# Kernel optimization log

Measured on AMD Instinct MI355X. Metric: run time of the kernel, lower is better.

## Reference

```python
import jax, jax.numpy as jnp
import numpy as np

NB_CLASSES = 1024
SZ_EMBED = 128
N_SAMPLES = 262144
MRG = 0.1
ALPHA = 32.0


def l2_norm(x):
    # matches torch l2_norm: divide by sqrt(sum(x^2, dim=1) + 1e-12)
    return x / jnp.sqrt(jnp.sum(x * x, axis=1, keepdims=True) + 1e-12)


def setup_inputs() -> dict:
    key = jax.random.key(0)
    k1, k2, k3 = jax.random.split(key, 3)
    X = jax.random.normal(k1, (N_SAMPLES, SZ_EMBED), dtype=jnp.float32)
    proxies = jax.random.normal(k2, (NB_CLASSES, SZ_EMBED), dtype=jnp.float32)
    T = jax.random.randint(k3, (N_SAMPLES,), 0, NB_CLASSES)
    return {"X": X, "proxies": proxies, "T": T}


def reference(X, proxies, T):
    # cosine similarities: [N, C]
    cos = l2_norm(X) @ l2_norm(proxies).T
    # on-device one-hot replaces the numpy binarize roundtrip
    P_one_hot = jax.nn.one_hot(T, NB_CLASSES, dtype=cos.dtype)  # [N, C]
    pos_exp_w = jnp.exp(-ALPHA * (cos - MRG)) * P_one_hot
    neg_exp_w = jnp.exp(ALPHA * (cos + MRG)) * (1.0 - P_one_hot)
    P_sim_sum = pos_exp_w.sum(axis=0)  # [C]
    N_sim_sum = neg_exp_w.sum(axis=0)  # [C]
    num_valid = (P_one_hot.sum(axis=0) != 0).sum().astype(cos.dtype)
    pos_term = jnp.where(
        num_valid > 0,
        jnp.log1p(P_sim_sum).sum() / jnp.maximum(num_valid, 1.0),
        jnp.zeros((), cos.dtype),
    )
    neg_term = jnp.log1p(N_sim_sum).sum() / NB_CLASSES
    loss = pos_term + neg_term
    return jnp.stack([loss, pos_term, neg_term])
```

## Files before the change

kernel.cpp:

```cpp
#include <hip/hip_runtime.h>
#include <math.h>

#define NB_CLASSES 1024
#define SZ_EMBED 128
#define N_SAMPLES 262144
#define MTILE 64
#define CTILE 64
#define NBLOCKS (N_SAMPLES / MTILE)
#define XSTRIDE 136

typedef __bf16 v8bf __attribute__((ext_vector_type(8)));
typedef float v4f __attribute__((ext_vector_type(4)));

#define EXP_A 46.16624130844683f
#define EXP_B 4.616624130844683f

#define SMEM_BYTES 36096

__device__ __forceinline__ unsigned short f2bf(float f) {
    union { float f; unsigned u; } v; v.f = f;
    unsigned u = v.u;
    unsigned rounding = 0x7FFFu + ((u >> 16) & 1u);
    return (unsigned short)((u + rounding) >> 16);
}
__device__ __forceinline__ float bfbits_lo(unsigned u) {
    union { unsigned u; float f; } v; v.u = u << 16; return v.f;
}
__device__ __forceinline__ float bfbits_hi(unsigned u) {
    union { unsigned u; float f; } v; v.u = u & 0xffff0000u; return v.f;
}

__global__ __launch_bounds__(256) void norm_proxies_kernel(
    const float* __restrict__ proxies, unsigned short* __restrict__ pn,
    float* __restrict__ pg) {
    if (blockIdx.x < 8) pg[blockIdx.x * 256 + threadIdx.x] = 0.f;
    int wv = threadIdx.x >> 6;
    int lane = threadIdx.x & 63;
    int row = blockIdx.x * 4 + wv;
    const float* src = proxies + (size_t)row * SZ_EMBED + lane * 2;
    float2 x = *(const float2*)src;
    float ss = x.x * x.x + x.y * x.y;
    #pragma unroll
    for (int off = 32; off; off >>= 1) ss += __shfl_xor(ss, off);
    float inv = rsqrtf(ss + 1e-12f);
    unsigned pk = (unsigned)f2bf(x.x * inv) | ((unsigned)f2bf(x.y * inv) << 16);
    *(unsigned*)(pn + (size_t)row * SZ_EMBED + lane * 2) = pk;
}

__global__ __launch_bounds__(256) void main_kernel(
    const float* __restrict__ X, const int* __restrict__ T,
    const unsigned short* __restrict__ Pn,
    float* __restrict__ partial_neg, float* __restrict__ pos_g,
    float* __restrict__ negd_g) {
    __shared__ __align__(16) char smem[SMEM_BYTES];
    unsigned short* xtile = (unsigned short*)smem;
    float (*psum)[4] = (float(*)[4])(smem + 17408);
    float (*dsum)[4] = (float(*)[4])(smem + 18432);
    int* tT = (int*)(smem + 19456);

    const int t = threadIdx.x;
    const int lane = t & 63;
    const int wv = t >> 6;
    const int quad = lane >> 4;
    const int l15 = lane & 15;
    const int sample_base = blockIdx.x * MTILE;
    const int row = t >> 2, part = t & 3;
    const char* PnB = (const char*)Pn;

#define STAGE(tc, b) do {                                                      \
        char* lb_ = smem + ((b) ? 0 : 19712) + wv * 4096;                      \
        _Pragma("unroll")                                                      \
        for (int c_ = 0; c_ < 4; ++c_) {                                       \
            int rw_ = c_ * 4 + (lane >> 4);                                    \
            const char* g_ = PnB + ((size_t)((tc) * 64 + wv * 16 + rw_)) * 256 \
                             + (((lane & 15) * 16) ^ ((rw_ & 7) << 4));        \
            __builtin_amdgcn_global_load_lds(                                  \
                (__attribute__((address_space(1))) const void*)g_,             \
                (__attribute__((address_space(3))) void*)(lb_ + c_ * 1024),    \
                16, 0, 0);                                                     \
        }                                                                      \
    } while (0)

    STAGE(0, 0);

    {
        const float4* src = (const float4*)(X + (size_t)(sample_base + row) * SZ_EMBED + part * 32);
        float4 r[8];
        float ss = 0.f;
        #pragma unroll
        for (int j = 0; j < 8; ++j) {
            r[j] = src[j];
            ss += r[j].x * r[j].x + r[j].y * r[j].y + r[j].z * r[j].z + r[j].w * r[j].w;
        }
        psum[row][part] = ss;
        if (t < MTILE) tT[t] = T[sample_base + t];
        __syncthreads();
        float inv = rsqrtf(psum[row][0] + psum[row][1] + psum[row][2] + psum[row][3] + 1e-12f);
        unsigned short* dst = xtile + row * XSTRIDE + part * 32;
        #pragma unroll
        for (int j = 0; j < 8; ++j) {
            uint2 pk;
            pk.x = (unsigned)f2bf(r[j].x * inv) | ((unsigned)f2bf(r[j].y * inv) << 16);
            pk.y = (unsigned)f2bf(r[j].z * inv) | ((unsigned)f2bf(r[j].w * inv) << 16);
            *(uint2*)(dst + j * 4) = pk;
        }
        int lbl = tT[row];
        const unsigned short* prow = Pn + (size_t)lbl * SZ_EMBED + part * 32;
        float d = 0.f;
        #pragma unroll
        for (int j = 0; j < 4; ++j) {
            uint4 pv = *(const uint4*)(prow + j * 8);
            float4 xa = r[2 * j], xb = r[2 * j + 1];
            d += bfbits_lo(pv.x) * xa.x + bfbits_hi(pv.x) * xa.y;
            d += bfbits_lo(pv.y) * xa.z + bfbits_hi(pv.y) * xa.w;
            d += bfbits_lo(pv.z) * xb.x + bfbits_hi(pv.z) * xb.y;
            d += bfbits_lo(pv.w) * xb.z + bfbits_hi(pv.w) * xb.w;
        }
        dsum[row][part] = d * inv;
        __syncthreads();
        if (part == 0) {
            int lbl2 = tT[row];
            float dd = dsum[row][0] + dsum[row][1] + dsum[row][2] + dsum[row][3];
            float dp = __builtin_amdgcn_exp2f(fmaf(dd, -EXP_A, EXP_B));
            float dn = __builtin_amdgcn_exp2f(fmaf(dd,  EXP_A, EXP_B));
            atomicAdd(&pos_g[lbl2], dp);
            atomicAdd(&negd_g[lbl2], dn);
        }
    }

    v8bf afrag[4][4];
    #pragma unroll
    for (int ri = 0; ri < 4; ++ri)
        #pragma unroll
        for (int kc = 0; kc < 4; ++kc)
            afrag[ri][kc] = *(const v8bf*)(xtile + (ri * 16 + l15) * XSTRIDE + kc * 32 + quad * 8);

    __syncthreads();

    float* nrow = partial_neg + (size_t)blockIdx.x * NB_CLASSES + wv * 16 + l15;
    const int bswz = ((l15 & 7) << 4);
    const int browoff = (wv * 16 + l15) * 256;

    #pragma unroll
    for (int ct = 0; ct < NB_CLASSES / CTILE; ++ct) {
        const int cur = ct & 1;
        if (ct < NB_CLASSES / CTILE - 1) STAGE(ct + 1, cur ^ 1);

        const char* bbase = smem + (cur ? 0 : 19712) + browoff;
        v8bf bfrag[4];
        #pragma unroll
        for (int kc = 0; kc < 4; ++kc)
            bfrag[kc] = *(const v8bf*)(bbase + ((kc * 64 + quad * 16) ^ bswz));

        v4f zero = {0.f, 0.f, 0.f, 0.f};
        v4f acc[4] = {zero, zero, zero, zero};
        #pragma unroll
        for (int kc = 0; kc < 4; ++kc)
            #pragma unroll
            for (int ri = 0; ri < 4; ++ri)
                acc[ri] = __builtin_amdgcn_mfma_f32_16x16x32_bf16(afrag[ri][kc], bfrag[kc], acc[ri], 0, 0, 0);

        float e[16];
        #pragma unroll
        for (int ri = 0; ri < 4; ++ri)
            #pragma unroll
            for (int r = 0; r < 4; ++r)
                e[ri * 4 + r] = __builtin_amdgcn_exp2f(fmaf(acc[ri][r], EXP_A, EXP_B));
        #pragma unroll
        for (int s = 8; s; s >>= 1)
            #pragma unroll
            for (int j = 0; j < s; ++j)
                e[j] += e[j + s];
        float v = e[0];
        v += __shfl_xor(v, 16);
        v += __shfl_xor(v, 32);
        if (quad == 0) nrow[ct * CTILE] = v;

        __syncthreads();
    }
#undef STAGE
}

__global__ __launch_bounds__(256) void row_reduce_kernel(float* __restrict__ partial_neg) {
    const int t = threadIdx.x;
    const int g = blockIdx.x >> 2, q = blockIdx.x & 3;
    float* base = partial_neg + (size_t)g * 64 * NB_CLASSES + q * 256 + t;
    float s = 0.f;
    #pragma unroll 8
    for (int r = 0; r < 64; ++r) s += base[(size_t)r * NB_CLASSES];
    base[0] = s;
}

__global__ __launch_bounds__(256) void finalize_kernel(
    const float* __restrict__ partial_neg, const float* __restrict__ pos_g,
    const float* __restrict__ negd_g, float* __restrict__ out) {
    int t = threadIdx.x;
    float4 ns = {0.f, 0.f, 0.f, 0.f};
    #pragma unroll 8
    for (int r = 0; r < 64; ++r) {
        float4 vn = *(const float4*)(partial_neg + (size_t)r * 64 * NB_CLASSES + 4 * t);
        ns.x += vn.x; ns.y += vn.y; ns.z += vn.z; ns.w += vn.w;
    }
    float4 nd = *(const float4*)(negd_g + 4 * t);
    ns.x -= nd.x; ns.y -= nd.y; ns.z -= nd.z; ns.w -= nd.w;
    float4 ps = *(const float4*)(pos_g + 4 * t);
    float lp_pos = log1pf(ps.x) + log1pf(ps.y) + log1pf(ps.z) + log1pf(ps.w);
    float lp_neg = log1pf(ns.x) + log1pf(ns.y) + log1pf(ns.z) + log1pf(ns.w);
    float valid = (ps.x != 0.f) + (ps.y != 0.f) + (ps.z != 0.f) + (ps.w != 0.f);
    #pragma unroll
    for (int off = 32; off; off >>= 1) {
        lp_pos += __shfl_xor(lp_pos, off);
        lp_neg += __shfl_xor(lp_neg, off);
        valid  += __shfl_xor(valid, off);
    }
    __shared__ float s[3][4];
    int wv = t >> 6, lane = t & 63;
    if (lane == 0) { s[0][wv] = lp_pos; s[1][wv] = lp_neg; s[2][wv] = valid; }
    __syncthreads();
    if (t == 0) {
        float P = s[0][0] + s[0][1] + s[0][2] + s[0][3];
        float Ng = s[1][0] + s[1][1] + s[1][2] + s[1][3];
        float V = s[2][0] + s[2][1] + s[2][2] + s[2][3];
        float pos_term = (V > 0.f) ? (P / fmaxf(V, 1.f)) : 0.f;
        float neg_term = Ng / (float)NB_CLASSES;
        out[0] = pos_term + neg_term;
        out[1] = pos_term;
        out[2] = neg_term;
    }
}

extern "C" void kernel_launch(void* const* d_in, const int* in_sizes, int n_in,
                              void* d_out, int out_size, void* d_ws, size_t ws_size,
                              hipStream_t stream) {
    const float* X = (const float*)d_in[0];
    const float* proxies = (const float*)d_in[1];
    const int* T = (const int*)d_in[2];
    float* out = (float*)d_out;

    char* ws = (char*)d_ws;
    unsigned short* Pn = (unsigned short*)ws;
    float* pos_g = (float*)(ws + (size_t)NB_CLASSES * SZ_EMBED * sizeof(unsigned short));
    float* negd_g = pos_g + NB_CLASSES;
    float* partial_neg = negd_g + NB_CLASSES;

    norm_proxies_kernel<<<NB_CLASSES / 4, 256, 0, stream>>>(proxies, Pn, pos_g);
    main_kernel<<<NBLOCKS, 256, 0, stream>>>(X, T, Pn, partial_neg, pos_g, negd_g);
    row_reduce_kernel<<<256, 256, 0, stream>>>(partial_neg);
    finalize_kernel<<<1, 256, 0, stream>>>(partial_neg, pos_g, negd_g, out);
}
```

Measured before the change: 289.1 us.

## Replace per-tile block barrier with vmcnt waits and pack exp-sum adds

Drops the __syncthreads at the end of each class-tile iteration. In its place, each wave waits on its own outstanding global loads with s_waitcnt vmcnt, and a sched_barrier keeps the compiler from moving code across that wait. The exponentials are now grouped into float2 vectors so the tree reduction can use packed fp32 adds, roughly halving the add instruction count. The change only stays correct if each wave stages and reads only its own part of the double-buffered LDS tile; otherwise removing the barrier opens a race between waves.

After: 283.8 us. No clear change (-1.8%).

```diff
diff --git a/kernel.cpp b/kernel.cpp
--- a/kernel.cpp
+++ b/kernel.cpp
@@ -11,6 +11,7 @@
 
 typedef __bf16 v8bf __attribute__((ext_vector_type(8)));
 typedef float v4f __attribute__((ext_vector_type(4)));
+typedef float v2f __attribute__((ext_vector_type(2)));
 
 #define EXP_A 46.16624130844683f
 #define EXP_B 4.616624130844683f
@@ -144,7 +145,13 @@
     #pragma unroll
     for (int ct = 0; ct < NB_CLASSES / CTILE; ++ct) {
         const int cur = ct & 1;
-        if (ct < NB_CLASSES / CTILE - 1) STAGE(ct + 1, cur ^ 1);
+        if (ct < NB_CLASSES / CTILE - 1) {
+            STAGE(ct + 1, cur ^ 1);
+            asm volatile("s_waitcnt vmcnt(4)" ::: "memory");
+        } else {
+            asm volatile("s_waitcnt vmcnt(0)" ::: "memory");
+        }
+        __builtin_amdgcn_sched_barrier(0);
 
         const char* bbase = smem + (cur ? 0 : 19712) + browoff;
         v8bf bfrag[4];
@@ -160,23 +167,25 @@
             for (int ri = 0; ri < 4; ++ri)
                 acc[ri] = __builtin_amdgcn_mfma_f32_16x16x32_bf16(afrag[ri][kc], bfrag[kc], acc[ri], 0, 0, 0);
 
-        float e[16];
-        #pragma unroll
-        for (int ri = 0; ri < 4; ++ri)
+        v2f e2[8];
+        #pragma unroll
+        for (int ri = 0; ri < 4; ++ri) {
+            float a0 = __builtin_amdgcn_exp2f(fmaf(acc[ri][0], EXP_A, EXP_B));
+            float a1 = __builtin_amdgcn_exp2f(fmaf(acc[ri][1], EXP_A, EXP_B));
+            float a2 = __builtin_amdgcn_exp2f(fmaf(acc[ri][2], EXP_A, EXP_B));
+            float a3 = __builtin_amdgcn_exp2f(fmaf(acc[ri][3], EXP_A, EXP_B));
+            e2[ri * 2]     = (v2f){a0, a1};
+            e2[ri * 2 + 1] = (v2f){a2, a3};
+        }
+        #pragma unroll
+        for (int s2 = 4; s2; s2 >>= 1)
             #pragma unroll
-            for (int r = 0; r < 4; ++r)
-                e[ri * 4 + r] = __builtin_amdgcn_exp2f(fmaf(acc[ri][r], EXP_A, EXP_B));
-        #pragma unroll
-        for (int s = 8; s; s >>= 1)
-            #pragma unroll
-            for (int j = 0; j < s; ++j)
-                e[j] += e[j + s];
-        float v = e[0];
+            for (int j = 0; j < s2; ++j)
+                e2[j] += e2[j + s2];
+        float v = e2[0].x + e2[0].y;
         v += __shfl_xor(v, 16);
         v += __shfl_xor(v, 32);
         if (quad == 0) nrow[ct * CTILE] = v;
-
-        __syncthreads();
     }
 #undef STAGE
 }
```

## Split warps 2x2 over rows/classes and move tile barrier before staging

Applied to the files above, without the earlier changes.

Each wave now computes a 32-row by 32-class sub-tile instead of all 64 rows by 16 classes, which halves the A-fragment registers per wave and doubles partial_neg rows per block. The row-reduce and finalize kernels are resized to the 128-row partial groups. The per-tile barrier moves to the start of the loop, preceded by an explicit vmcnt wait, and the exp-sum uses paired float adds. The intent is lower register pressure, better occupancy and less sync overhead, at the cost of twice as much partial-sum memory traffic.

New measurement: 299.4 us. 1.04x slower.

```diff
diff --git a/kernel.cpp b/kernel.cpp
--- a/kernel.cpp
+++ b/kernel.cpp
@@ -11,6 +11,7 @@
 
 typedef __bf16 v8bf __attribute__((ext_vector_type(8)));
 typedef float v4f __attribute__((ext_vector_type(4)));
+typedef float v2f __attribute__((ext_vector_type(2)));
 
 #define EXP_A 46.16624130844683f
 #define EXP_B 4.616624130844683f
@@ -63,6 +64,8 @@
     const int wv = t >> 6;
     const int quad = lane >> 4;
     const int l15 = lane & 15;
+    const int wr = wv >> 1;
+    const int wc = wv & 1;
     const int sample_base = blockIdx.x * MTILE;
     const int row = t >> 2, part = t & 3;
     const char* PnB = (const char*)Pn;
@@ -128,55 +131,59 @@
         }
     }
 
-    v8bf afrag[4][4];
-    #pragma unroll
-    for (int ri = 0; ri < 4; ++ri)
+    v8bf afrag[2][4];
+    #pragma unroll
+    for (int ri = 0; ri < 2; ++ri)
         #pragma unroll
         for (int kc = 0; kc < 4; ++kc)
-            afrag[ri][kc] = *(const v8bf*)(xtile + (ri * 16 + l15) * XSTRIDE + kc * 32 + quad * 8);
+            afrag[ri][kc] = *(const v8bf*)(xtile + (wr * 32 + ri * 16 + l15) * XSTRIDE + kc * 32 + quad * 8);
 
     __syncthreads();
 
-    float* nrow = partial_neg + (size_t)blockIdx.x * NB_CLASSES + wv * 16 + l15;
+    float* nrow = partial_neg + (size_t)(blockIdx.x * 2 + wr) * NB_CLASSES + wc * 32 + l15;
     const int bswz = ((l15 & 7) << 4);
-    const int browoff = (wv * 16 + l15) * 256;
+    const int brow0 = (wc * 32 + l15) * 256;
 
     #pragma unroll
     for (int ct = 0; ct < NB_CLASSES / CTILE; ++ct) {
         const int cur = ct & 1;
+        asm volatile("s_waitcnt vmcnt(2)" ::: "memory");
+        __builtin_amdgcn_s_barrier();
+        __builtin_amdgcn_sched_barrier(0);
         if (ct < NB_CLASSES / CTILE - 1) STAGE(ct + 1, cur ^ 1);
-
-        const char* bbase = smem + (cur ? 0 : 19712) + browoff;
-        v8bf bfrag[4];
-        #pragma unroll
-        for (int kc = 0; kc < 4; ++kc)
-            bfrag[kc] = *(const v8bf*)(bbase + ((kc * 64 + quad * 16) ^ bswz));
-
-        v4f zero = {0.f, 0.f, 0.f, 0.f};
-        v4f acc[4] = {zero, zero, zero, zero};
-        #pragma unroll
-        for (int kc = 0; kc < 4; ++kc)
+        __builtin_amdgcn_sched_barrier(0);
+
+        const char* bbase = smem + (cur ? 0 : 19712);
+        #pragma unroll
+        for (int ci = 0; ci < 2; ++ci) {
+            const char* bb = bbase + brow0 + ci * 4096;
+            v8bf bfrag[4];
             #pragma unroll
-            for (int ri = 0; ri < 4; ++ri)
-                acc[ri] = __builtin_amdgcn_mfma_f32_16x16x32_bf16(afrag[ri][kc], bfrag[kc], acc[ri], 0, 0, 0);
-
-        float e[16];
-        #pragma unroll
-        for (int ri = 0; ri < 4; ++ri)
+            for (int kc = 0; kc < 4; ++kc)
+                bfrag[kc] = *(const v8bf*)(bb + ((kc * 64 + quad * 16) ^ bswz));
+
+            v4f zero = {0.f, 0.f, 0.f, 0.f};
+            v4f a0 = zero, a1 = zero;
             #pragma unroll
-            for (int r = 0; r < 4; ++r)
-                e[ri * 4 + r] = __builtin_amdgcn_exp2f(fmaf(acc[ri][r], EXP_A, EXP_B));
-        #pragma unroll
-        for (int s = 8; s; s >>= 1)
-            #pragma unroll
-            for (int j = 0; j < s; ++j)
-                e[j] += e[j + s];
-        float v = e[0];
-        v += __shfl_xor(v, 16);
-        v += __shfl_xor(v, 32);
-        if (quad == 0) nrow[ct * CTILE] = v;
-
-        __syncthreads();
+            for (int kc = 0; kc < 4; ++kc) {
+                a0 = __builtin_amdgcn_mfma_f32_16x16x32_bf16(afrag[0][kc], bfrag[kc], a0, 0, 0, 0);
+                a1 = __builtin_amdgcn_mfma_f32_16x16x32_bf16(afrag[1][kc], bfrag[kc], a1, 0, 0, 0);
+            }
+            v2f p0, p1, p2, p3;
+            p0 = (v2f){__builtin_amdgcn_exp2f(fmaf(a0[0], EXP_A, EXP_B)),
+                       __builtin_amdgcn_exp2f(fmaf(a0[1], EXP_A, EXP_B))};
+            p1 = (v2f){__builtin_amdgcn_exp2f(fmaf(a0[2], EXP_A, EXP_B)),
+                       __builtin_amdgcn_exp2f(fmaf(a0[3], EXP_A, EXP_B))};
+            p2 = (v2f){__builtin_amdgcn_exp2f(fmaf(a1[0], EXP_A, EXP_B)),
+                       __builtin_amdgcn_exp2f(fmaf(a1[1], EXP_A, EXP_B))};
+            p3 = (v2f){__builtin_amdgcn_exp2f(fmaf(a1[2], EXP_A, EXP_B)),
+                       __builtin_amdgcn_exp2f(fmaf(a1[3], EXP_A, EXP_B))};
+            p0 += p2; p1 += p3; p0 += p1;
+            float v = p0.x + p0.y;
+            v += __shfl_xor(v, 16);
+            v += __shfl_xor(v, 32);
+            if (quad == 0) nrow[ct * CTILE + ci * 16] = v;
+        }
     }
 #undef STAGE
 }
@@ -184,10 +191,10 @@
 __global__ __launch_bounds__(256) void row_reduce_kernel(float* __restrict__ partial_neg) {
     const int t = threadIdx.x;
     const int g = blockIdx.x >> 2, q = blockIdx.x & 3;
-    float* base = partial_neg + (size_t)g * 64 * NB_CLASSES + q * 256 + t;
+    float* base = partial_neg + (size_t)g * 128 * NB_CLASSES + q * 256 + t;
     float s = 0.f;
     #pragma unroll 8
-    for (int r = 0; r < 64; ++r) s += base[(size_t)r * NB_CLASSES];
+    for (int r = 0; r < 128; ++r) s += base[(size_t)r * NB_CLASSES];
     base[0] = s;
 }
 
@@ -198,7 +205,7 @@
     float4 ns = {0.f, 0.f, 0.f, 0.f};
     #pragma unroll 8
     for (int r = 0; r < 64; ++r) {
-        float4 vn = *(const float4*)(partial_neg + (size_t)r * 64 * NB_CLASSES + 4 * t);
+        float4 vn = *(const float4*)(partial_neg + (size_t)r * 128 * NB_CLASSES + 4 * t);
         ns.x += vn.x; ns.y += vn.y; ns.z += vn.z; ns.w += vn.w;
     }
     float4 nd = *(const float4*)(negd_g + 4 * t);
```
